# Performance work log

Hardware: AMD Instinct MI355X
Metric: run time of the kernel (lower is better)

Reference implementation:

```python
import jax, jax.numpy as jnp
import numpy as np

V, E, U, L = 32000, 512, 1024, 2  # vocab, embed_dim, units, layers
B, T = 64, 256


def setup_inputs() -> dict:
    key = jax.random.key(0)
    ks = jax.random.split(key, 8)
    s = lambda k, shape: jax.random.normal(k, shape, jnp.float32) * 0.02
    return {
        "tokens": jax.random.randint(ks[0], (B, T), 0, V),
        "emb": s(ks[1], (V, E)),
        "W0": s(ks[2], (E, 4 * U)), "U0": s(ks[3], (U, 4 * U)),
        "b0": jnp.zeros((4 * U,), jnp.float32),
        "W1": s(ks[4], (U, 4 * U)), "U1": s(ks[5], (U, 4 * U)),
        "b1": jnp.zeros((4 * U,), jnp.float32),
    }


def _lstm_layer(x, W, Uw, b):
    # x: [B,T,D]. Precompute all input projections: [T,B,4U] (batched GEMM outside scan).
    xz = jnp.einsum('btd,dg->tbg', x, W) + b
    units = Uw.shape[0]

    def step(carry, xz_t):
        h, c = carry
        z = xz_t + h @ Uw  # [B,4U]
        i, f, g, o = jnp.split(z, 4, axis=-1)  # Keras gate order: i,f,c,o
        i = jax.nn.sigmoid(i)
        f = jax.nn.sigmoid(f)
        g = jnp.tanh(g)
        o = jax.nn.sigmoid(o)
        c = f * c + i * g
        h = o * jnp.tanh(c)
        return (h, c), h

    h0 = jnp.zeros((x.shape[0], units), x.dtype)
    (h, c), ys = jax.lax.scan(step, (h0, h0), xz)
    return jnp.transpose(ys, (1, 0, 2)), h, c  # [B,T,U], [B,U], [B,U]


def reference(tokens, emb, W0, U0, b0, W1, U1, b1):
    x = emb[tokens]  # [B,T,E] embedding lookup
    x, h, c = _lstm_layer(x, W0, U0, b0)
    x, h, c = _lstm_layer(x, W1, U1, b1)
    # Keras: return_sequences=True, return_state=True -> (seq, h_last, c_last) of last layer
    return (x, h, c)
```

## Files before the change

kernel.cpp:

```cpp
#include <hip/hip_runtime.h>


typedef _Float16 f16;
typedef _Float16 f16x8 __attribute__((ext_vector_type(8)));
typedef _Float16 f16x4 __attribute__((ext_vector_type(4)));
typedef float f32x4 __attribute__((ext_vector_type(4)));

__device__ __forceinline__ f32x4 mfma16x32(f16x8 a, f16x8 b, f32x4 c) {
  return __builtin_amdgcn_mfma_f32_16x16x32_f16(a, b, c, 0, 0, 0);
}

__device__ __forceinline__ void gl_lds16(const void* g, void* l) {
  __builtin_amdgcn_global_load_lds(
      (const __attribute__((address_space(1))) void*)g,
      (__attribute__((address_space(3))) void*)l, 16, 0, 0);
}

__device__ __forceinline__ float sigmoidf_(float x) {
  return 1.0f / (1.0f + expf(-x));
}

__device__ __forceinline__ void st_f16_sc(f16* p, float v) {
  f16 h = (f16)v;
  unsigned u = (unsigned)__builtin_bit_cast(unsigned short, h);
  asm volatile("global_store_short %0, %1, off sc0 sc1"
               :: "v"(p), "v"(u) : "memory");
}

__device__ __forceinline__ unsigned ld_flag(const unsigned* p) {
  return __hip_atomic_load(p, __ATOMIC_RELAXED, __HIP_MEMORY_SCOPE_AGENT);
}
__device__ __forceinline__ void st_flag(unsigned* p, unsigned v) {
  __hip_atomic_store(p, v, __ATOMIC_RELAXED, __HIP_MEMORY_SCOPE_AGENT);
}

__global__ __launch_bounds__(256) void k_transpose_f16(
    const float* __restrict__ S, f16* __restrict__ D, int K, int N) {
  __shared__ float tile[64][65];
  int nk = K >> 6;
  int k0 = (blockIdx.x % nk) << 6;
  int n0 = (blockIdx.x / nk) << 6;
  int tc = threadIdx.x & 63;
  int tq = threadIdx.x >> 6;
#pragma unroll
  for (int r = 0; r < 16; ++r) {
    int kk = tq * 16 + r;
    tile[kk][tc] = S[(size_t)(k0 + kk) * N + (n0 + tc)];
  }
  __syncthreads();
#pragma unroll
  for (int r = 0; r < 16; ++r) {
    int nn = tq * 16 + r;
    D[(size_t)(n0 + nn) * K + (k0 + tc)] = (f16)tile[tc][nn];
  }
}

__global__ __launch_bounds__(256) void k_embed_f16(
    const int* __restrict__ tok, const float* __restrict__ emb,
    f16* __restrict__ A0) {
  int i = blockIdx.x * 256 + threadIdx.x;
  int m = i >> 7;
  int e = (i & 127) << 2;
  int t = m >> 6, b = m & 63;
  int tk = tok[b * 256 + t];
  const float4 v = *(const float4*)(emb + (size_t)tk * 512 + e);
  f16x4 o = {(f16)v.x, (f16)v.y, (f16)v.z, (f16)v.w};
  *(f16x4*)(A0 + (size_t)m * 512 + e) = o;
}

__global__ __launch_bounds__(256) void k_gemm_f16(
    const f16* __restrict__ A, const f16* __restrict__ Bt,
    const float* __restrict__ bias, f16* __restrict__ C,
    int M, int N, int K) {
  __shared__ f16 sA[2][128 * 32];
  __shared__ f16 sB[2][128 * 32];
  const int tid = threadIdx.x, lane = tid & 63, w = tid >> 6;
  const int mb = M >> 7;
  const int bm = blockIdx.x % mb, bn = blockIdx.x / mb;
  const int am0 = bm << 7, bn0 = bn << 7;
  const int wm = w >> 1, wn = w & 1;
  const int srow = lane >> 2, sch = lane & 3;

  f32x4 acc[4][4] = {};
  const int NT = K >> 5;
  int cur = 0;

  auto stage = [&](int kt, int buf) {
#pragma unroll
    for (int q2 = 0; q2 < 2; ++q2) {
      int q = w * 2 + q2;
      int row = q * 16 + srow;
      const f16* ga = A + (size_t)(am0 + row) * K + kt * 32 + sch * 8;
      const f16* gb = Bt + (size_t)(bn0 + row) * K + kt * 32 + sch * 8;
      gl_lds16(ga, (char*)&sA[buf][0] + q * 1024);
      gl_lds16(gb, (char*)&sB[buf][0] + q * 1024);
    }
  };

  stage(0, 0);
  __syncthreads();
  for (int kt = 0; kt < NT; ++kt) {
    if (kt + 1 < NT) stage(kt + 1, cur ^ 1);
    const f16* pa = &sA[cur][(wm * 64 + (lane & 15)) * 32 + (lane >> 4) * 8];
    const f16* pb = &sB[cur][(wn * 64 + (lane & 15)) * 32 + (lane >> 4) * 8];
    f16x8 av[4], bv[4];
#pragma unroll
    for (int mf = 0; mf < 4; ++mf) av[mf] = *(const f16x8*)(pa + mf * 512);
#pragma unroll
    for (int nf = 0; nf < 4; ++nf) bv[nf] = *(const f16x8*)(pb + nf * 512);
#pragma unroll
    for (int mf = 0; mf < 4; ++mf)
#pragma unroll
      for (int nf = 0; nf < 4; ++nf)
        acc[mf][nf] = mfma16x32(av[mf], bv[nf], acc[mf][nf]);
    __syncthreads();
    cur ^= 1;
  }

#pragma unroll
  for (int mf = 0; mf < 4; ++mf)
#pragma unroll
    for (int nf = 0; nf < 4; ++nf) {
      int col = bn0 + wn * 64 + nf * 16 + (lane & 15);
      float bs = bias[col];
#pragma unroll
      for (int r = 0; r < 4; ++r) {
        int row = am0 + wm * 64 + mf * 16 + (lane >> 4) * 4 + r;
        C[(size_t)row * N + col] = (f16)(acc[mf][nf][r] + bs);
      }
    }
}

__global__ __launch_bounds__(256, 2) void k_scan6(
    const f16* __restrict__ XZ, const f16* __restrict__ U0t,
    const f16* __restrict__ W1t, const f16* __restrict__ U1t,
    const float* __restrict__ b1, f16* __restrict__ A1,
    f16* __restrict__ H1h, float* __restrict__ out, unsigned* arr0,
    unsigned* rel0, unsigned* arr1, unsigned* rel1, unsigned* mir) {
  __shared__ float zred[4608];
  const int tid = threadIdx.x, lane = tid & 63, w = tid >> 6;
  const bool isL1 = (blockIdx.x >= 256);
  const int rb = isL1 ? (int)blockIdx.x - 256 : (int)blockIdx.x;
  const int ug = ((rb & 7) << 4) + ((rb >> 3) & 15);
  const int rh = rb >> 7;
  const int u0 = ug * 8;
  const int j = lane & 15, kg = lane >> 4;
  const int aoff = (rh * 32 + j) * 1024 + w * 256 + kg * 8;
  const int erl = tid >> 3;
  const int eunit = tid & 7;
  const int q_e = eunit >> 2, euu = eunit & 3;
  const int erow = rh * 32 + erl;
  const int eu = u0 + eunit;

  const int wo0 = ((j >> 2) * 1024 + u0 + (j & 3)) * 1024 + w * 256 + kg * 8;
  const int wo1 = wo0 + 4 * 1024;
  f16x8 bA0[8], bA1[8], bB0[8], bB1[8];
  {
    const f16* base = isL1 ? W1t : U0t;
#pragma unroll
    for (int kt = 0; kt < 8; ++kt) {
      bA0[kt] = *(const f16x8*)(base + wo0 + kt * 32);
      bA1[kt] = *(const f16x8*)(base + wo1 + kt * 32);
      asm volatile("" : "+v"(bA0[kt]), "+v"(bA1[kt]));
    }
  }
  if (isL1) {
#pragma unroll
    for (int kt = 0; kt < 8; ++kt) {
      bB0[kt] = *(const f16x8*)(U1t + wo0 + kt * 32);
      bB1[kt] = *(const f16x8*)(U1t + wo1 + kt * 32);
      asm volatile("" : "+v"(bB0[kt]), "+v"(bB1[kt]));
    }
  }
  float c = 0.0f;

  if (!isL1) {
    float xz[4];
#pragma unroll
    for (int g = 0; g < 4; ++g)
      xz[g] = (float)XZ[(size_t)erow * 4096 + g * 1024 + eu];

    for (int s = 0; s < 256; ++s) {
      f32x4 a0[2] = {}, a1[2] = {};
      if (s > 0) {
        const f16* ap = A1 + (size_t)(s - 1) * 65536 + aoff;
#pragma unroll
        for (int kt = 0; kt < 8; ++kt)
#pragma unroll
          for (int mf = 0; mf < 2; ++mf) {
            f16x8 av = *(const f16x8*)(ap + mf * 16384 + kt * 32);
            a0[mf] = mfma16x32(av, bA0[kt], a0[mf]);
            a1[mf] = mfma16x32(av, bA1[kt], a1[mf]);
          }
      }
#pragma unroll
      for (int mf = 0; mf < 2; ++mf)
#pragma unroll
        for (int r = 0; r < 4; ++r) {
          zred[w * 576 + (mf * 16 + kg * 4 + r) * 18 + j] = a0[mf][r];
          zred[2304 + w * 576 + (mf * 16 + kg * 4 + r) * 18 + j] = a1[mf][r];
        }
      __syncthreads();
      float z[4];
#pragma unroll
      for (int g = 0; g < 4; ++g) {
        float sm = xz[g];
#pragma unroll
        for (int wv = 0; wv < 4; ++wv)
          sm += zred[q_e * 2304 + wv * 576 + erl * 18 + g * 4 + euu];
        z[g] = sm;
      }
      float gi = sigmoidf_(z[0]), gf = sigmoidf_(z[1]);
      float gg = tanhf(z[2]), go = sigmoidf_(z[3]);
      c = gf * c + gi * gg;
      st_f16_sc(&A1[(size_t)(s * 64 + erow) * 1024 + eu], go * tanhf(c));

      asm volatile("s_waitcnt vmcnt(0)" ::: "memory");
      float xzn[4] = {0.f, 0.f, 0.f, 0.f};
      if (s + 1 < 256) {
        const f16* xrow = XZ + (size_t)((s + 1) * 64 + erow) * 4096;
#pragma unroll
        for (int g = 0; g < 4; ++g) xzn[g] = (float)xrow[g * 1024 + eu];
      }
      __syncthreads();

      const unsigned v = (unsigned)s + 1u;
      if (rb == 0) {
        if (tid > 0) {
          while (ld_flag(&arr0[(unsigned)tid * 32u]) < v)
            __builtin_amdgcn_s_sleep(1);
        }
        __syncthreads();
        if (tid > 0) st_flag(&rel0[(unsigned)tid * 32u], v);
        st_flag(&mir[(unsigned)tid * 32u], v);
      } else {
        if (tid == 0) {
          st_flag(&arr0[(unsigned)rb * 32u], v);
          while (ld_flag(&rel0[(unsigned)rb * 32u]) < v)
            __builtin_amdgcn_s_sleep(1);
        }
        __syncthreads();
      }
#pragma unroll
      for (int g = 0; g < 4; ++g) xz[g] = xzn[g];
    }
  } else {
    float bias1[4];
#pragma unroll
    for (int g = 0; g < 4; ++g) bias1[g] = b1[g * 1024 + eu];

    if (tid == 0) {
      while (ld_flag(&mir[(unsigned)rb * 32u]) < 1u)
        __builtin_amdgcn_s_sleep(1);
    }
    __syncthreads();
    f32x4 accW0[2] = {}, accW1[2] = {};
    {
      const f16* ap = A1 + aoff;
#pragma unroll
      for (int kt = 0; kt < 8; ++kt)
#pragma unroll
        for (int mf = 0; mf < 2; ++mf) {
          f16x8 av = *(const f16x8*)(ap + mf * 16384 + kt * 32);
          accW0[mf] = mfma16x32(av, bA0[kt], accW0[mf]);
          accW1[mf] = mfma16x32(av, bA1[kt], accW1[mf]);
        }
    }

    for (int t = 0; t < 256; ++t) {
      f32x4 a0[2] = {accW0[0], accW0[1]};
      f32x4 a1[2] = {accW1[0], accW1[1]};
      if (t > 0) {
        const f16* hp = H1h + (size_t)(t - 1) * 65536 + aoff;
#pragma unroll
        for (int kt = 0; kt < 8; ++kt)
#pragma unroll
          for (int mf = 0; mf < 2; ++mf) {
            f16x8 av = *(const f16x8*)(hp + mf * 16384 + kt * 32);
            a0[mf] = mfma16x32(av, bB0[kt], a0[mf]);
            a1[mf] = mfma16x32(av, bB1[kt], a1[mf]);
          }
      }
#pragma unroll
      for (int mf = 0; mf < 2; ++mf)
#pragma unroll
        for (int r = 0; r < 4; ++r) {
          zred[w * 576 + (mf * 16 + kg * 4 + r) * 18 + j] = a0[mf][r];
          zred[2304 + w * 576 + (mf * 16 + kg * 4 + r) * 18 + j] = a1[mf][r];
        }
      __syncthreads();
      float z[4];
#pragma unroll
      for (int g = 0; g < 4; ++g) {
        float sm = bias1[g];
#pragma unroll
        for (int wv = 0; wv < 4; ++wv)
          sm += zred[q_e * 2304 + wv * 576 + erl * 18 + g * 4 + euu];
        z[g] = sm;
      }
      float gi = sigmoidf_(z[0]), gf = sigmoidf_(z[1]);
      float gg = tanhf(z[2]), go = sigmoidf_(z[3]);
      c = gf * c + gi * gg;
      float hn = go * tanhf(c);
      if (t == 255) {
        out[(size_t)erow * 262144 + (size_t)t * 1024 + eu] = hn;
        out[16777216 + erow * 1024 + eu] = hn;
        out[16777216 + 65536 + erow * 1024 + eu] = c;
        break;
      }
      st_f16_sc(&H1h[(size_t)t * 65536 + erow * 1024 + eu], hn);

      asm volatile("s_waitcnt vmcnt(0)" ::: "memory");
      __syncthreads();
      const unsigned v = (unsigned)t + 1u;
      if (rb == 0) {
        if (tid > 0) {
          while (ld_flag(&arr1[(unsigned)tid * 32u]) < v)
            __builtin_amdgcn_s_sleep(1);
        }
        __syncthreads();
        if (tid > 0) st_flag(&rel1[(unsigned)tid * 32u], v);
      } else {
        if (tid == 0) st_flag(&arr1[(unsigned)rb * 32u], v);
      }
      out[(size_t)erow * 262144 + (size_t)t * 1024 + eu] = hn;
      if (tid == 0) {
        while (ld_flag(&mir[(unsigned)rb * 32u]) < v + 1u)
          __builtin_amdgcn_s_sleep(1);
      }
      __syncthreads();
      {
        const f16* ap = A1 + (size_t)(t + 1) * 65536 + aoff;
        f32x4 t0[2] = {}, t1[2] = {};
#pragma unroll
        for (int kt = 0; kt < 8; ++kt)
#pragma unroll
          for (int mf = 0; mf < 2; ++mf) {
            f16x8 av = *(const f16x8*)(ap + mf * 16384 + kt * 32);
            t0[mf] = mfma16x32(av, bA0[kt], t0[mf]);
            t1[mf] = mfma16x32(av, bA1[kt], t1[mf]);
          }
#pragma unroll
        for (int mf = 0; mf < 2; ++mf) {
          accW0[mf] = t0[mf];
          accW1[mf] = t1[mf];
        }
      }
      if (rb != 0) {
        if (tid == 0) {
          while (ld_flag(&rel1[(unsigned)rb * 32u]) < v)
            __builtin_amdgcn_s_sleep(1);
        }
        __syncthreads();
      }
    }
  }
}

__device__ __forceinline__ void reduce4(const f32x4 acc[4], float* zred,
                                        float z[4]) {
  const int tid = threadIdx.x, lane = tid & 63, w = tid >> 6;
  const int j = lane & 15, kg = lane >> 4;
#pragma unroll
  for (int mf = 0; mf < 4; ++mf)
#pragma unroll
    for (int r = 0; r < 4; ++r)
      zred[w * 1088 + (mf * 16 + kg * 4 + r) * 17 + j] = acc[mf][r];
  __syncthreads();
  const int erow = tid >> 2, euu = tid & 3;
#pragma unroll
  for (int g = 0; g < 4; ++g) {
#pragma unroll
    for (int wv = 0; wv < 4; ++wv)
      z[g] += zred[wv * 1088 + erow * 17 + g * 4 + euu];
  }
}

__device__ __forceinline__ void step_once(
    int s, int u0, const f16x8 bvU0[8], const f16x8 bvW1[8],
    const f16x8 bvU1[8], const float bias1[4], const float xz[4],
    f16* __restrict__ A1, f16* __restrict__ H1h, int hmask,
    float& c0, float& c1, float* __restrict__ out, float* zred) {
  const int tid = threadIdx.x, lane = tid & 63, w = tid >> 6;
  const int j = lane & 15, kg = lane >> 4;
  const int aoff = j * 1024 + w * 256 + kg * 8;
  const int erow = tid >> 2;
  const int eu = u0 + (tid & 3);

  f32x4 accA[4] = {};
  f32x4 accB[4] = {};

  if (s >= 1) {
    const f16* ap = A1 + (size_t)(s - 1) * 65536 + aoff;
#pragma unroll
    for (int kt = 0; kt < 8; ++kt)
#pragma unroll
      for (int mf = 0; mf < 4; ++mf) {
        f16x8 av = *(const f16x8*)(ap + mf * 16384 + kt * 32);
        if (s < 256) accA[mf] = mfma16x32(av, bvU0[kt], accA[mf]);
        accB[mf] = mfma16x32(av, bvW1[kt], accB[mf]);
      }
    if (s >= 2) {
      const f16* hp = H1h + (size_t)((s - 2) & hmask) * 65536 + aoff;
#pragma unroll
      for (int kt = 0; kt < 8; ++kt)
#pragma unroll
        for (int mf = 0; mf < 4; ++mf)
          accB[mf] = mfma16x32(*(const f16x8*)(hp + mf * 16384 + kt * 32),
                               bvU1[kt], accB[mf]);
    }
  }

  if (s < 256) {
    float z[4] = {xz[0], xz[1], xz[2], xz[3]};
    reduce4(accA, zred, z);
    float gi = sigmoidf_(z[0]), gf = sigmoidf_(z[1]);
    float gg = tanhf(z[2]), go = sigmoidf_(z[3]);
    c0 = gf * c0 + gi * gg;
    st_f16_sc(&A1[(size_t)(s * 64 + erow) * 1024 + eu], go * tanhf(c0));
  }
  __syncthreads();

  if (s >= 1) {
    const int t = s - 1;
    float z[4] = {bias1[0], bias1[1], bias1[2], bias1[3]};
    reduce4(accB, zred, z);
    float gi = sigmoidf_(z[0]), gf = sigmoidf_(z[1]);
    float gg = tanhf(z[2]), go = sigmoidf_(z[3]);
    c1 = gf * c1 + gi * gg;
    float hn = go * tanhf(c1);
    st_f16_sc(&H1h[(size_t)(t & hmask) * 65536 + erow * 1024 + eu], hn);
    out[(size_t)erow * 262144 + (size_t)t * 1024 + eu] = hn;
    if (t == 255) {
      out[16777216 + erow * 1024 + eu] = hn;
      out[16777216 + 65536 + erow * 1024 + eu] = c1;
    }
  }
}

__global__ __launch_bounds__(256, 1) void k_step(
    const f16* __restrict__ XZ, const f16* __restrict__ U0t,
    const f16* __restrict__ W1t, const f16* __restrict__ U1t,
    const float* __restrict__ b1, f16* __restrict__ A1,
    f16* __restrict__ H1h, float* __restrict__ C0, float* __restrict__ C1,
    float* __restrict__ out, int s) {
  __shared__ float zred[4352];
  const int tid_ = threadIdx.x, lane_ = tid_ & 63, w_ = tid_ >> 6;
  const int bid_ = (int)blockIdx.x;
  const int i_ = ((bid_ & 7) << 5) + (bid_ >> 3);
  const int u0 = i_ * 4;
  const int j_ = lane_ & 15;
  const int kg_ = lane_ >> 4;
  const int ncol_ = (j_ >> 2) * 1024 + u0 + (j_ & 3);
  const int woff_ = ncol_ * 1024 + w_ * 256 + kg_ * 8;
  f16x8 bvU0[8], bvW1[8], bvU1[8];
#pragma unroll
  for (int kt = 0; kt < 8; ++kt) {
    bvU0[kt] = *(const f16x8*)(U0t + woff_ + kt * 32);
    bvW1[kt] = *(const f16x8*)(W1t + woff_ + kt * 32);
    bvU1[kt] = *(const f16x8*)(U1t + woff_ + kt * 32);
  }
  const int erow_ = tid_ >> 2;
  const int eu_ = u0 + (tid_ & 3);
  float bias1[4];
#pragma unroll
  for (int g = 0; g < 4; ++g) bias1[g] = b1[g * 1024 + eu_];

  float xz[4] = {0.f, 0.f, 0.f, 0.f};
  if (s < 256) {
    const f16* xrow = XZ + (size_t)(s * 64 + erow_) * 4096;
#pragma unroll
    for (int g = 0; g < 4; ++g) xz[g] = (float)xrow[g * 1024 + eu_];
  }
  float c0 = C0[erow_ * 1024 + eu_];
  float c1 = C1[erow_ * 1024 + eu_];
  step_once(s, u0, bvU0, bvW1, bvU1, bias1, xz, A1, H1h, 1, c0, c1, out,
            zred);
  C0[erow_ * 1024 + eu_] = c0;
  C1[erow_ * 1024 + eu_] = c1;
}

extern "C" void kernel_launch(void* const* d_in, const int* in_sizes, int n_in,
                              void* d_out, int out_size, void* d_ws, size_t ws_size,
                              hipStream_t stream) {
  (void)in_sizes; (void)n_in; (void)out_size;
  const int* tokens = (const int*)d_in[0];
  const float* emb = (const float*)d_in[1];
  const float* W0 = (const float*)d_in[2];
  const float* U0 = (const float*)d_in[3];
  const float* b0 = (const float*)d_in[4];
  const float* W1 = (const float*)d_in[5];
  const float* U1 = (const float*)d_in[6];
  const float* b1 = (const float*)d_in[7];
  float* out = (float*)d_out;

  char* p = (char*)d_ws;
  f16* A0 = (f16*)p;   p += (size_t)16384 * 512 * 2;
  f16* A1 = (f16*)p;   p += (size_t)16384 * 1024 * 2;
  f16* W0t = (f16*)p;  p += (size_t)4096 * 512 * 2;
  f16* U0t = (f16*)p;  p += (size_t)4096 * 1024 * 2;
  f16* W1t = (f16*)p;  p += (size_t)4096 * 1024 * 2;
  f16* U1t = (f16*)p;  p += (size_t)4096 * 1024 * 2;
  f16* XZ = (f16*)p;   p += (size_t)16384 * 4096 * 2;
  float* C0 = (float*)p; p += 64 * 1024 * 4;
  float* C1 = (float*)p; p += 64 * 1024 * 4;
  unsigned* arr0 = (unsigned*)p; p += 256 * 32 * 4;
  unsigned* rel0 = (unsigned*)p; p += 256 * 32 * 4;
  unsigned* arr1 = (unsigned*)p; p += 256 * 32 * 4;
  unsigned* rel1 = (unsigned*)p; p += 256 * 32 * 4;
  unsigned* mir = (unsigned*)p; p += 256 * 32 * 4;
  f16* H1h = (f16*)p;
  const size_t need_coop = (size_t)(p - (char*)d_ws) + (size_t)256 * 65536 * 2;

  k_transpose_f16<<<512, 256, 0, stream>>>(W0, W0t, 512, 4096);
  k_transpose_f16<<<1024, 256, 0, stream>>>(U0, U0t, 1024, 4096);
  k_transpose_f16<<<1024, 256, 0, stream>>>(W1, W1t, 1024, 4096);
  k_transpose_f16<<<1024, 256, 0, stream>>>(U1, U1t, 1024, 4096);

  k_embed_f16<<<8192, 256, 0, stream>>>(tokens, emb, A0);

  k_gemm_f16<<<4096, 256, 0, stream>>>(A0, W0t, b0, XZ, 16384, 4096, 512);

  hipMemsetAsync(C0, 0, 64 * 1024 * 4 * 2, stream);
  hipMemsetAsync(arr0, 0, 5 * 256 * 32 * 4, stream);

  bool coop_ok = (ws_size >= need_coop);
  if (coop_ok) {
    const f16* XZc = XZ; const f16* U0c = U0t; const f16* W1c = W1t;
    const f16* U1c = U1t; const float* b1c = b1;
    f16* A1p = A1; f16* H1p = H1h; float* outp = out;
    unsigned* a0 = arr0; unsigned* r0 = rel0;
    unsigned* a1 = arr1; unsigned* r1 = rel1; unsigned* mr = mir;
    void* kargs[] = {(void*)&XZc, (void*)&U0c, (void*)&W1c, (void*)&U1c,
                     (void*)&b1c, (void*)&A1p, (void*)&H1p, (void*)&outp,
                     (void*)&a0, (void*)&r0, (void*)&a1, (void*)&r1,
                     (void*)&mr};
    hipError_t e = hipLaunchCooperativeKernel((const void*)k_scan6, dim3(512),
                                              dim3(256), kargs, 0, stream);
    if (e != hipSuccess) {
      (void)hipGetLastError();
      coop_ok = false;
    }
  }
  if (!coop_ok) {
    for (int s = 0; s <= 256; ++s)
      k_step<<<256, 256, 0, stream>>>(XZ, U0t, W1t, U1t, b1, A1, H1h, C0, C1,
                                      out, s);
  }
}
```

Measured before the change: 2.416 ms.

## Split scan barriers per batch half and coalesce hidden-state stores

The per-step grid barrier is split into independent groups for each batch half (rh) and each layer. Each group has its own master block, so the two batch halves no longer synchronise with each other. Hidden-state outputs are staged in LDS and written as one 16-byte store per row instead of scattered 2-byte stores. The asm register-pinning barriers on the weight fragments are also removed. In exchange, each step gains an extra __syncthreads, and each 128-block group now relies on its own flag layout being correct.

```diff
diff --git a/kernel.cpp b/kernel.cpp
--- a/kernel.cpp
+++ b/kernel.cpp
@@ -25,6 +25,10 @@
   unsigned u = (unsigned)__builtin_bit_cast(unsigned short, h);
   asm volatile("global_store_short %0, %1, off sc0 sc1"
                :: "v"(p), "v"(u) : "memory");
+}
+__device__ __forceinline__ void st_b128_sc(f16* p, f16x8 v) {
+  asm volatile("global_store_dwordx4 %0, %1, off sc0 sc1"
+               :: "v"(p), "v"(v) : "memory");
 }
 
 __device__ __forceinline__ unsigned ld_flag(const unsigned* p) {
@@ -131,18 +135,20 @@
     }
 }
 
-__global__ __launch_bounds__(256, 2) void k_scan6(
+__global__ __launch_bounds__(256, 2) void k_scan7(
     const f16* __restrict__ XZ, const f16* __restrict__ U0t,
     const f16* __restrict__ W1t, const f16* __restrict__ U1t,
     const float* __restrict__ b1, f16* __restrict__ A1,
-    f16* __restrict__ H1h, float* __restrict__ out, unsigned* arr0,
-    unsigned* rel0, unsigned* arr1, unsigned* rel1, unsigned* mir) {
+    f16* __restrict__ H1h, float* __restrict__ out, unsigned* arr,
+    unsigned* rel, unsigned* mir) {
   __shared__ float zred[4608];
+  __shared__ f16 hstage[32][8];
   const int tid = threadIdx.x, lane = tid & 63, w = tid >> 6;
   const bool isL1 = (blockIdx.x >= 256);
   const int rb = isL1 ? (int)blockIdx.x - 256 : (int)blockIdx.x;
   const int ug = ((rb & 7) << 4) + ((rb >> 3) & 15);
   const int rh = rb >> 7;
+  const int cid = rb & 127;
   const int u0 = ug * 8;
   const int j = lane & 15, kg = lane >> 4;
   const int aoff = (rh * 32 + j) * 1024 + w * 256 + kg * 8;
@@ -151,6 +157,9 @@
   const int q_e = eunit >> 2, euu = eunit & 3;
   const int erow = rh * 32 + erl;
   const int eu = u0 + eunit;
+  unsigned* gArr = arr + (size_t)(((isL1 ? 2 : 0) + rh) * 128) * 32;
+  unsigned* gRel = rel + (size_t)(((isL1 ? 2 : 0) + rh) * 128) * 32;
+  unsigned* gMir = mir + (size_t)(rh * 128) * 32;
 
   const int wo0 = ((j >> 2) * 1024 + u0 + (j & 3)) * 1024 + w * 256 + kg * 8;
   const int wo1 = wo0 + 4 * 1024;
@@ -161,7 +170,6 @@
     for (int kt = 0; kt < 8; ++kt) {
       bA0[kt] = *(const f16x8*)(base + wo0 + kt * 32);
       bA1[kt] = *(const f16x8*)(base + wo1 + kt * 32);
-      asm volatile("" : "+v"(bA0[kt]), "+v"(bA1[kt]));
     }
   }
   if (isL1) {
@@ -169,7 +177,6 @@
     for (int kt = 0; kt < 8; ++kt) {
       bB0[kt] = *(const f16x8*)(U1t + wo0 + kt * 32);
       bB1[kt] = *(const f16x8*)(U1t + wo1 + kt * 32);
-      asm volatile("" : "+v"(bB0[kt]), "+v"(bB1[kt]));
     }
   }
   float c = 0.0f;
@@ -213,7 +220,11 @@
       float gi = sigmoidf_(z[0]), gf = sigmoidf_(z[1]);
       float gg = tanhf(z[2]), go = sigmoidf_(z[3]);
       c = gf * c + gi * gg;
-      st_f16_sc(&A1[(size_t)(s * 64 + erow) * 1024 + eu], go * tanhf(c));
+      hstage[erl][eunit] = (f16)(go * tanhf(c));
+      __syncthreads();
+      if (tid < 32)
+        st_b128_sc(&A1[(size_t)(s * 64 + rh * 32 + tid) * 1024 + u0],
+                   *(const f16x8*)hstage[tid]);
 
       asm volatile("s_waitcnt vmcnt(0)" ::: "memory");
       float xzn[4] = {0.f, 0.f, 0.f, 0.f};
@@ -225,18 +236,18 @@
       __syncthreads();
 
       const unsigned v = (unsigned)s + 1u;
-      if (rb == 0) {
-        if (tid > 0) {
-          while (ld_flag(&arr0[(unsigned)tid * 32u]) < v)
+      if (cid == 0) {
+        if (tid >= 1 && tid < 128) {
+          while (ld_flag(&gArr[(unsigned)tid * 32u]) < v)
             __builtin_amdgcn_s_sleep(1);
         }
         __syncthreads();
-        if (tid > 0) st_flag(&rel0[(unsigned)tid * 32u], v);
-        st_flag(&mir[(unsigned)tid * 32u], v);
+        if (tid >= 1 && tid < 128) st_flag(&gRel[(unsigned)tid * 32u], v);
+        if (tid < 128) st_flag(&gMir[(unsigned)tid * 32u], v);
       } else {
         if (tid == 0) {
-          st_flag(&arr0[(unsigned)rb * 32u], v);
-          while (ld_flag(&rel0[(unsigned)rb * 32u]) < v)
+          st_flag(&gArr[(unsigned)cid * 32u], v);
+          while (ld_flag(&gRel[(unsigned)cid * 32u]) < v)
             __builtin_amdgcn_s_sleep(1);
         }
         __syncthreads();
@@ -250,7 +261,7 @@
     for (int g = 0; g < 4; ++g) bias1[g] = b1[g * 1024 + eu];
 
     if (tid == 0) {
-      while (ld_flag(&mir[(unsigned)rb * 32u]) < 1u)
+      while (ld_flag(&gMir[(unsigned)cid * 32u]) < 1u)
         __builtin_amdgcn_s_sleep(1);
     }
     __syncthreads();
@@ -308,24 +319,28 @@
         out[16777216 + 65536 + erow * 1024 + eu] = c;
         break;
       }
-      st_f16_sc(&H1h[(size_t)t * 65536 + erow * 1024 + eu], hn);
+      hstage[erl][eunit] = (f16)hn;
+      __syncthreads();
+      if (tid < 32)
+        st_b128_sc(&H1h[(size_t)t * 65536 + (rh * 32 + tid) * 1024 + u0],
+                   *(const f16x8*)hstage[tid]);
 
       asm volatile("s_waitcnt vmcnt(0)" ::: "memory");
       __syncthreads();
       const unsigned v = (unsigned)t + 1u;
-      if (rb == 0) {
-        if (tid > 0) {
-          while (ld_flag(&arr1[(unsigned)tid * 32u]) < v)
+      if (cid == 0) {
+        if (tid >= 1 && tid < 128) {
+          while (ld_flag(&gArr[(unsigned)tid * 32u]) < v)
             __builtin_amdgcn_s_sleep(1);
         }
         __syncthreads();
-        if (tid > 0) st_flag(&rel1[(unsigned)tid * 32u], v);
+        if (tid >= 1 && tid < 128) st_flag(&gRel[(unsigned)tid * 32u], v);
       } else {
-        if (tid == 0) st_flag(&arr1[(unsigned)rb * 32u], v);
+        if (tid == 0) st_flag(&gArr[(unsigned)cid * 32u], v);
       }
       out[(size_t)erow * 262144 + (size_t)t * 1024 + eu] = hn;
       if (tid == 0) {
-        while (ld_flag(&mir[(unsigned)rb * 32u]) < v + 1u)
+        while (ld_flag(&gMir[(unsigned)cid * 32u]) < v + 1u)
           __builtin_amdgcn_s_sleep(1);
       }
       __syncthreads();
@@ -346,9 +361,9 @@
           accW1[mf] = t1[mf];
         }
       }
-      if (rb != 0) {
+      if (cid != 0) {
         if (tid == 0) {
-          while (ld_flag(&rel1[(unsigned)rb * 32u]) < v)
+          while (ld_flag(&gRel[(unsigned)cid * 32u]) < v)
             __builtin_amdgcn_s_sleep(1);
         }
         __syncthreads();
@@ -504,11 +519,9 @@
   f16* XZ = (f16*)p;   p += (size_t)16384 * 4096 * 2;
   float* C0 = (float*)p; p += 64 * 1024 * 4;
   float* C1 = (float*)p; p += 64 * 1024 * 4;
-  unsigned* arr0 = (unsigned*)p; p += 256 * 32 * 4;
-  unsigned* rel0 = (unsigned*)p; p += 256 * 32 * 4;
-  unsigned* arr1 = (unsigned*)p; p += 256 * 32 * 4;
-  unsigned* rel1 = (unsigned*)p; p += 256 * 32 * 4;
-  unsigned* mir = (unsigned*)p; p += 256 * 32 * 4;
+  unsigned* arr = (unsigned*)p; p += 4 * 128 * 32 * 4;
+  unsigned* rel = (unsigned*)p; p += 4 * 128 * 32 * 4;
+  unsigned* mir = (unsigned*)p; p += 2 * 128 * 32 * 4;
   f16* H1h = (f16*)p;
   const size_t need_coop = (size_t)(p - (char*)d_ws) + (size_t)256 * 65536 * 2;
 
@@ -522,20 +535,18 @@
   k_gemm_f16<<<4096, 256, 0, stream>>>(A0, W0t, b0, XZ, 16384, 4096, 512);
 
   hipMemsetAsync(C0, 0, 64 * 1024 * 4 * 2, stream);
-  hipMemsetAsync(arr0, 0, 5 * 256 * 32 * 4, stream);
+  hipMemsetAsync(arr, 0, 10 * 128 * 32 * 4, stream);
 
   bool coop_ok = (ws_size >= need_coop);
   if (coop_ok) {
     const f16* XZc = XZ; const f16* U0c = U0t; const f16* W1c = W1t;
     const f16* U1c = U1t; const float* b1c = b1;
     f16* A1p = A1; f16* H1p = H1h; float* outp = out;
-    unsigned* a0 = arr0; unsigned* r0 = rel0;
-    unsigned* a1 = arr1; unsigned* r1 = rel1; unsigned* mr = mir;
+    unsigned* ar = arr; unsigned* rl = rel; unsigned* mr = mir;
     void* kargs[] = {(void*)&XZc, (void*)&U0c, (void*)&W1c, (void*)&U1c,
                      (void*)&b1c, (void*)&A1p, (void*)&H1p, (void*)&outp,
-                     (void*)&a0, (void*)&r0, (void*)&a1, (void*)&r1,
-                     (void*)&mr};
-    hipError_t e = hipLaunchCooperativeKernel((const void*)k_scan6, dim3(512),
+                     (void*)&ar, (void*)&rl, (void*)&mr};
+    hipError_t e = hipLaunchCooperativeKernel((const void*)k_scan7, dim3(512),
                                               dim3(256), kargs, 0, stream);
     if (e != hipSuccess) {
       (void)hipGetLastError();
```

Result: faster. 2.233 ms (-7.6%).
